# Kernel tuning notes

Hardware: AMD Instinct MI355X
Metric: run time of the kernel (lower is better)

The kernel has to match this reference:

```python
import jax, jax.numpy as jnp
import numpy as np
from jax import lax

N = 100000      # nodes
F_IN = 128      # dataset.num_features
H = 64          # hidden
E = 1600000     # edges
G = 1000        # graphs (equal-sized, contiguous)
PER = N // G    # nodes per graph = 100
K = 30          # sort-pool k
KS = 3          # conv1d kernel = num_layers


def setup_inputs() -> dict:
    key = jax.random.key(0)
    ks = jax.random.split(key, 20)
    lin = lambda k, i, o: (jax.random.normal(k, (i, o), jnp.float32) / np.sqrt(i)).astype(jnp.float32)
    return {
        "x": jax.random.normal(ks[0], (N, F_IN), jnp.float32),
        "src": jax.random.randint(ks[1], (E,), 0, N, dtype=jnp.int32),
        "dst": jax.random.randint(ks[2], (E,), 0, N, dtype=jnp.int32),
        "num_graphs": G,
        # SAGEConv 1: lin_l (aggr, with bias), lin_r (self, no bias)
        "wl1": lin(ks[3], F_IN, H), "wr1": lin(ks[4], F_IN, H), "b1": jnp.zeros((H,), jnp.float32),
        "wl2": lin(ks[5], H, H), "wr2": lin(ks[6], H, H), "b2": jnp.zeros((H,), jnp.float32),
        "wl3": lin(ks[7], H, H), "wr3": lin(ks[8], H, H), "b3": jnp.zeros((H,), jnp.float32),
        # Conv1d(hidden=64 -> 32, kernel=3): weight [O, I, K]
        "cw": (jax.random.normal(ks[9], (32, H, KS), jnp.float32) / np.sqrt(H * KS)).astype(jnp.float32),
        "cb": jnp.zeros((32,), jnp.float32),
        "w1": lin(ks[10], 32 * (K - KS + 1), H), "bb1": jnp.zeros((H,), jnp.float32),
        "w2": lin(ks[11], H, 1), "bb2": jnp.zeros((1,), jnp.float32),
    }


def _sage(x, src, dst, wl, wr, b, n):
    # PyG SAGEConv (mean aggr): lin_l(mean_{j->i} x_j) + lin_r(x_i)
    msum = jax.ops.segment_sum(x[src], dst, num_segments=n)           # [N, F]
    cnt = jax.ops.segment_sum(jnp.ones((src.shape[0],), x.dtype), dst, num_segments=n)
    mean = msum / jnp.maximum(cnt, 1.0)[:, None]
    return mean @ wl + b + x @ wr


def reference(x, src, dst, num_graphs, wl1, wr1, b1, wl2, wr2, b2, wl3, wr3, b3, cw, cb, w1, bb1, w2, bb2):
    n = x.shape[0]
    h = jax.nn.relu(_sage(x, src, dst, wl1, wr1, b1, n))
    h = jax.nn.relu(_sage(h, src, dst, wl2, wr2, b2, n))
    h = jax.nn.relu(_sage(h, src, dst, wl3, wr3, b3, n))
    # SortAggregation(k): per-graph, sort nodes by last feature channel (desc), keep top-k.
    # batch = contiguous equal-sized graphs -> dense reshape is exact.
    hg = h.reshape(num_graphs, PER, H)                                # [G, PER, H]
    order = jnp.argsort(-hg[:, :, -1], axis=1)[:, :K]                 # [G, K]
    topk = jnp.take_along_axis(hg, order[:, :, None], axis=1)         # [G, K, H]
    xc = jnp.transpose(topk, (0, 2, 1))                               # [G, H, K]
    y = lax.conv_general_dilated(xc, cw, (1,), 'VALID',
                                 dimension_numbers=('NCH', 'OIH', 'NCH'))
    y = jax.nn.relu(y + cb[None, :, None])                            # [G, 32, K-KS+1]
    y = y.reshape(num_graphs, -1)
    y = jax.nn.relu(y @ w1 + bb1)
    # dropout: eval mode -> identity
    return y @ w2 + bb2                                               # [G, 1]
```

## Files before the change

### kernel.cpp

```cpp
#include <hip/hip_runtime.h>

#define NN 100000
#define EE 1600000
#define GG 1000
#define PERG 100
#define KK 30
#define HH 64

#define NB 782
#define CAP 4096
#define CHB 4096
#define BUCKET_BLOCKS ((EE + CHB - 1) / CHB)
#define PROJ_BLOCKS ((NN + 127) / 128)

__global__ __launch_bounds__(1024) void zero_int(int* p, int n) {
  int i = blockIdx.x * 1024 + threadIdx.x;
  if (i < n) p[i] = 0;
}

__device__ __forceinline__ void bucket_body(int bid, float* smem,
                                            const int* __restrict__ src,
                                            const int* __restrict__ dst,
                                            int* __restrict__ gcur,
                                            int* __restrict__ pairs) {
  int* lhist = (int*)smem;
  int* lbase = lhist + NB;
  int* lcur = lbase + NB;
  const int t = threadIdx.x;
  const int c0 = bid * CHB;
  const int c1 = min(c0 + CHB, EE);
  for (int b = t; b < NB; b += 256) {
    lhist[b] = 0;
    lcur[b] = 0;
  }
  __syncthreads();
  for (int e = c0 + t; e < c1; e += 256) atomicAdd(&lhist[dst[e] >> 7], 1);
  __syncthreads();
  for (int b = t; b < NB; b += 256) {
    int c = lhist[b];
    lbase[b] = c ? atomicAdd(&gcur[b], c) : 0;
  }
  __syncthreads();
  for (int e = c0 + t; e < c1; e += 256) {
    int d = dst[e];
    int b = d >> 7;
    int p = atomicAdd(&lcur[b], 1);
    pairs[b * CAP + lbase[b] + p] = (src[e] << 7) | (d & 127);
  }
}

template <int K>
__device__ __forceinline__ void proj_body(int bid, float* smem,
                                          const float* __restrict__ X,
                                          const float* __restrict__ WL,
                                          const float* __restrict__ WR,
                                          float* __restrict__ P,
                                          float* __restrict__ R) {
  constexpr int BM = 128, BK = 32, XSP = 40, WSP = 144;
  float* xs = smem;
  float* ws = smem + BM * XSP;
  const int t = threadIdx.x;
  const int row0 = bid * BM;
  const int tc = t & 15, tr = t >> 4;
  const int wcol = tc * 8 + (tc >> 2) * 4;

  float acc[8][8];
#pragma unroll
  for (int i = 0; i < 8; ++i)
#pragma unroll
    for (int j = 0; j < 8; ++j) acc[i][j] = 0.f;

  for (int k0 = 0; k0 < K; k0 += BK) {
    __syncthreads();
    for (int idx = t; idx < BM * 8; idx += 256) {
      int r = idx >> 3, c = idx & 7;
      int row = row0 + r;
      float4 v = make_float4(0.f, 0.f, 0.f, 0.f);
      if (row < NN) v = *reinterpret_cast<const float4*>(&X[(size_t)row * K + k0 + c * 4]);
      *reinterpret_cast<float4*>(&xs[r * XSP + c * 4]) = v;
    }
    for (int idx = t; idx < BK * 16; idx += 256) {
      int kr = idx >> 4, c4 = idx & 15;
      int gcl = c4 >> 1;
      int off = gcl * 8 + (gcl >> 2) * 4 + (c4 & 1) * 4;
      *reinterpret_cast<float4*>(&ws[kr * WSP + off]) =
          *reinterpret_cast<const float4*>(&WL[(k0 + kr) * 64 + c4 * 4]);
      int g2 = gcl + 8;
      int off2 = g2 * 8 + (g2 >> 2) * 4 + (c4 & 1) * 4;
      *reinterpret_cast<float4*>(&ws[kr * WSP + off2]) =
          *reinterpret_cast<const float4*>(&WR[(k0 + kr) * 64 + c4 * 4]);
    }
    __syncthreads();
    for (int kk4 = 0; kk4 < BK; kk4 += 4) {
      float4 a[8];
#pragma unroll
      for (int i = 0; i < 8; ++i)
        a[i] = *reinterpret_cast<const float4*>(&xs[(tr + 16 * i) * XSP + kk4]);
#pragma unroll
      for (int kk = 0; kk < 4; ++kk) {
        float4 b0 = *reinterpret_cast<const float4*>(&ws[(kk4 + kk) * WSP + wcol]);
        float4 b1 = *reinterpret_cast<const float4*>(&ws[(kk4 + kk) * WSP + wcol + 4]);
        float bv[8] = {b0.x, b0.y, b0.z, b0.w, b1.x, b1.y, b1.z, b1.w};
#pragma unroll
        for (int i = 0; i < 8; ++i) {
          float av = (kk == 0) ? a[i].x : (kk == 1) ? a[i].y : (kk == 2) ? a[i].z : a[i].w;
#pragma unroll
          for (int j = 0; j < 8; ++j) acc[i][j] = fmaf(av, bv[j], acc[i][j]);
        }
      }
    }
  }

  float* OUT = (tc < 8) ? P : R;
  int cb = (tc & 7) * 8;
#pragma unroll
  for (int i = 0; i < 8; ++i) {
    int row = row0 + tr + 16 * i;
    if (row < NN) {
      *reinterpret_cast<float4*>(&OUT[(size_t)row * 64 + cb]) =
          make_float4(acc[i][0], acc[i][1], acc[i][2], acc[i][3]);
      *reinterpret_cast<float4*>(&OUT[(size_t)row * 64 + cb + 4]) =
          make_float4(acc[i][4], acc[i][5], acc[i][6], acc[i][7]);
    }
  }
}

__global__ __launch_bounds__(256) void fused_bucket_proj(const int* __restrict__ src,
                                                         const int* __restrict__ dst,
                                                         int* __restrict__ gcur,
                                                         int* __restrict__ pairs,
                                                         const float* __restrict__ X,
                                                         const float* __restrict__ WL,
                                                         const float* __restrict__ WR,
                                                         float* __restrict__ P,
                                                         float* __restrict__ R) {
  __shared__ float smem[128 * 40 + 32 * 144];
  if (blockIdx.x < BUCKET_BLOCKS)
    bucket_body(blockIdx.x, smem, src, dst, gcur, pairs);
  else
    proj_body<128>(blockIdx.x - BUCKET_BLOCKS, smem, X, WL, WR, P, R);
}

template <int K>
__global__ __launch_bounds__(256) void proj_kernel(const float* __restrict__ X,
                                                   const float* __restrict__ WL,
                                                   const float* __restrict__ WR,
                                                   float* __restrict__ P,
                                                   float* __restrict__ R) {
  __shared__ float smem[128 * 40 + 32 * 144];
  proj_body<K>(blockIdx.x, smem, X, WL, WR, P, R);
}

__global__ __launch_bounds__(256) void csr_kernel(const int* __restrict__ gcur,
                                                  const int* __restrict__ pairs,
                                                  int* __restrict__ row_start,
                                                  int* __restrict__ cnt,
                                                  int* __restrict__ eidx) {
  __shared__ int vals[CAP];
  __shared__ int hist[128];
  __shared__ int offs[128];
  __shared__ int cur[128];
  __shared__ int red[4];
  const int b = blockIdx.x;
  const int t = threadIdx.x;
  int s = 0;
  for (int i = t; i < b; i += 256) s += gcur[i];
#pragma unroll
  for (int off = 32; off > 0; off >>= 1) s += __shfl_xor(s, off);
  if ((t & 63) == 0) red[t >> 6] = s;
  if (t < 128) {
    hist[t] = 0;
    cur[t] = 0;
  }
  __syncthreads();
  const int base = red[0] + red[1] + red[2] + red[3];
  const int nb = gcur[b];
  for (int i = t; i < nb; i += 256) {
    int v = pairs[b * CAP + i];
    vals[i] = v;
    atomicAdd(&hist[v & 127], 1);
  }
  __syncthreads();
  if (t < 128) {
    int ss = 0;
    for (int m = 0; m < t; ++m) ss += hist[m];
    offs[t] = ss;
    int node = b * 128 + t;
    if (node < NN) {
      row_start[node] = base + ss;
      cnt[node] = hist[t];
    }
  }
  __syncthreads();
  for (int i = t; i < nb; i += 256) {
    int v = vals[i];
    int ld = v & 127;
    int p = atomicAdd(&cur[ld], 1);
    eidx[base + offs[ld] + p] = v >> 7;
  }
}

__global__ __launch_bounds__(256) void agg_kernel(const float* __restrict__ P,
                                                  const float* __restrict__ R,
                                                  const float* __restrict__ bias,
                                                  const int* __restrict__ row_start,
                                                  const int* __restrict__ cnt,
                                                  const int* __restrict__ eidx,
                                                  float* __restrict__ h,
                                                  float* __restrict__ keys) {
  int wid = (blockIdx.x * 256 + threadIdx.x) >> 6;
  int lane = threadIdx.x & 63;
  if (wid >= NN) return;
  const int q = lane >> 4;
  const int ql = lane & 15;
  const int base = row_start[wid];
  const int deg = cnt[wid];
  float4 a0 = make_float4(0.f, 0.f, 0.f, 0.f);
  float4 a1 = make_float4(0.f, 0.f, 0.f, 0.f);

  for (int e0 = 0; e0 < deg; e0 += 64) {
    const int m = min(64, deg - e0);
    int idx = (lane < m) ? eidx[base + e0 + lane] : 0;
    for (int j = 0; j < m; j += 16) {
      const int eA = j + q, eB = j + 4 + q, eC = j + 8 + q, eD = j + 12 + q;
      const int sA = __shfl(idx, min(eA, m - 1));
      const int sB = __shfl(idx, min(eB, m - 1));
      const int sC = __shfl(idx, min(eC, m - 1));
      const int sD = __shfl(idx, min(eD, m - 1));
      const float wA = (eA < m) ? 1.f : 0.f;
      const float wB = (eB < m) ? 1.f : 0.f;
      const float wC = (eC < m) ? 1.f : 0.f;
      const float wD = (eD < m) ? 1.f : 0.f;
      float4 vA = *reinterpret_cast<const float4*>(&P[(size_t)sA * 64 + ql * 4]);
      float4 vB = *reinterpret_cast<const float4*>(&P[(size_t)sB * 64 + ql * 4]);
      float4 vC = *reinterpret_cast<const float4*>(&P[(size_t)sC * 64 + ql * 4]);
      float4 vD = *reinterpret_cast<const float4*>(&P[(size_t)sD * 64 + ql * 4]);
      a0.x = fmaf(wA, vA.x, a0.x); a0.y = fmaf(wA, vA.y, a0.y);
      a0.z = fmaf(wA, vA.z, a0.z); a0.w = fmaf(wA, vA.w, a0.w);
      a1.x = fmaf(wB, vB.x, a1.x); a1.y = fmaf(wB, vB.y, a1.y);
      a1.z = fmaf(wB, vB.z, a1.z); a1.w = fmaf(wB, vB.w, a1.w);
      a0.x = fmaf(wC, vC.x, a0.x); a0.y = fmaf(wC, vC.y, a0.y);
      a0.z = fmaf(wC, vC.z, a0.z); a0.w = fmaf(wC, vC.w, a0.w);
      a1.x = fmaf(wD, vD.x, a1.x); a1.y = fmaf(wD, vD.y, a1.y);
      a1.z = fmaf(wD, vD.z, a1.z); a1.w = fmaf(wD, vD.w, a1.w);
    }
  }

  float4 acc = make_float4(a0.x + a1.x, a0.y + a1.y, a0.z + a1.z, a0.w + a1.w);
#pragma unroll
  for (int d = 16; d < 64; d <<= 1) {
    acc.x += __shfl_xor(acc.x, d);
    acc.y += __shfl_xor(acc.y, d);
    acc.z += __shfl_xor(acc.z, d);
    acc.w += __shfl_xor(acc.w, d);
  }

  if (q == 0) {
    const float dv = fmaxf((float)deg, 1.0f);
    float4 r4 = *reinterpret_cast<const float4*>(&R[(size_t)wid * 64 + ql * 4]);
    float4 b4 = *reinterpret_cast<const float4*>(&bias[ql * 4]);
    float4 o;
    o.x = fmaxf(acc.x / dv + b4.x + r4.x, 0.f);
    o.y = fmaxf(acc.y / dv + b4.y + r4.y, 0.f);
    o.z = fmaxf(acc.z / dv + b4.z + r4.z, 0.f);
    o.w = fmaxf(acc.w / dv + b4.w + r4.w, 0.f);
    *reinterpret_cast<float4*>(&h[(size_t)wid * 64 + ql * 4]) = o;
    if (keys != nullptr && ql == 15) keys[wid] = o.w;
  }
}

__global__ __launch_bounds__(256) void head_kernel(const float* __restrict__ h,
                                                   const float* __restrict__ keysArr,
                                                   const float* __restrict__ cw,
                                                   const float* __restrict__ cb,
                                                   const float* __restrict__ w1,
                                                   const float* __restrict__ bb1,
                                                   const float* __restrict__ w2,
                                                   const float* __restrict__ bb2,
                                                   float* __restrict__ out) {
  __shared__ float key[PERG];
  __shared__ int sel[KK];
  __shared__ float feat[34 * 65];
  __shared__ float cwT[192 * 33];
  __shared__ float z[896];
  __shared__ float psum[256];
  const int g = blockIdx.x;
  const int t = threadIdx.x;

  for (int idx = t; idx < 32 * 192; idx += 256) {
    int o = idx / 192, k = idx % 192;
    cwT[k * 33 + o] = cw[idx];
  }
  if (t < PERG) key[t] = keysArr[g * PERG + t];
  __syncthreads();

  if (t < PERG) {
    float kv = key[t];
    int r = 0;
    for (int m = 0; m < PERG; ++m) {
      float km = key[m];
      r += (int)((km > kv) || (km == kv && m < t));
    }
    if (r < KK) sel[r] = t;
  }
  __syncthreads();

  for (int idx = t; idx < KK * HH; idx += 256) {
    int r = idx >> 6, f = idx & 63;
    feat[r * 65 + f] = h[(size_t)(g * PERG + sel[r]) * HH + f];
  }
  __syncthreads();

  {
    const int o = t & 31;
    const int pg = t >> 5;
    float zacc[4] = {0.f, 0.f, 0.f, 0.f};
    int i = 0, tt = 0;
    for (int k = 0; k < 192; ++k) {
      float c = cwT[k * 33 + o];
#pragma unroll
      for (int j = 0; j < 4; ++j) {
        int p = pg + 8 * j;
        zacc[j] = fmaf(c, feat[(p + tt) * 65 + i], zacc[j]);
      }
      if (++tt == 3) {
        tt = 0;
        ++i;
      }
    }
    float cbo = cb[o];
#pragma unroll
    for (int j = 0; j < 4; ++j) {
      int p = pg + 8 * j;
      if (p < 28) z[o * 28 + p] = fmaxf(zacc[j] + cbo, 0.f);
    }
  }
  __syncthreads();

  {
    const int hh = t & 63;
    const int quarter = t >> 6;
    const int q0 = quarter * 224;
    float acc = 0.f;
    for (int q = 0; q < 224; ++q)
      acc = fmaf(z[q0 + q], w1[(size_t)(q0 + q) * 64 + hh], acc);
    psum[t] = acc;
  }
  __syncthreads();

  if (t < 64) {
    float o1 = fmaxf(bb1[t] + psum[t] + psum[t + 64] + psum[t + 128] + psum[t + 192], 0.f);
    float v = o1 * w2[t];
#pragma unroll
    for (int off = 32; off > 0; off >>= 1) v += __shfl_down(v, off);
    if (t == 0) out[g] = v + bb2[0];
  }
}

extern "C" void kernel_launch(void* const* d_in, const int* in_sizes, int n_in,
                              void* d_out, int out_size, void* d_ws, size_t ws_size,
                              hipStream_t stream) {
  const float* x = (const float*)d_in[0];
  const int* src = (const int*)d_in[1];
  const int* dst = (const int*)d_in[2];
  const float* wl1 = (const float*)d_in[4];
  const float* wr1 = (const float*)d_in[5];
  const float* b1 = (const float*)d_in[6];
  const float* wl2 = (const float*)d_in[7];
  const float* wr2 = (const float*)d_in[8];
  const float* b2 = (const float*)d_in[9];
  const float* wl3 = (const float*)d_in[10];
  const float* wr3 = (const float*)d_in[11];
  const float* b3 = (const float*)d_in[12];
  const float* cw = (const float*)d_in[13];
  const float* cb = (const float*)d_in[14];
  const float* w1 = (const float*)d_in[15];
  const float* bb1 = (const float*)d_in[16];
  const float* w2 = (const float*)d_in[17];
  const float* bb2 = (const float*)d_in[18];
  float* out = (float*)d_out;

  char* w = (char*)d_ws;
  auto carve = [&](size_t bytes) {
    char* p = w;
    w += (bytes + 255) & ~(size_t)255;
    return p;
  };
  int* row_start = (int*)carve((size_t)NN * 4);
  int* cnt = (int*)carve((size_t)NN * 4);
  int* eidx = (int*)carve((size_t)EE * 4);
  float* P = (float*)carve((size_t)NN * 64 * 4);
  float* R = (float*)carve((size_t)NN * 64 * 4);
  float* hbuf = (float*)carve((size_t)NN * 64 * 4);
  float* keys = (float*)carve((size_t)NN * 4);
  int* gcur = (int*)carve((size_t)NB * 4);
  int* pairs = (int*)hbuf;

  zero_int<<<1, 1024, 0, stream>>>(gcur, NB);
  fused_bucket_proj<<<BUCKET_BLOCKS + PROJ_BLOCKS, 256, 0, stream>>>(
      src, dst, gcur, pairs, x, wl1, wr1, P, R);
  csr_kernel<<<NB, 256, 0, stream>>>(gcur, pairs, row_start, cnt, eidx);

  const int aggGrid = (NN + 3) / 4;
  agg_kernel<<<aggGrid, 256, 0, stream>>>(P, R, b1, row_start, cnt, eidx, hbuf, nullptr);
  proj_kernel<64><<<PROJ_BLOCKS, 256, 0, stream>>>(hbuf, wl2, wr2, P, R);
  agg_kernel<<<aggGrid, 256, 0, stream>>>(P, R, b2, row_start, cnt, eidx, hbuf, nullptr);
  proj_kernel<64><<<PROJ_BLOCKS, 256, 0, stream>>>(hbuf, wl3, wr3, P, R);
  agg_kernel<<<aggGrid, 256, 0, stream>>>(P, R, b3, row_start, cnt, eidx, hbuf, keys);
  head_kernel<<<GG, 256, 0, stream>>>(hbuf, keys, cw, cb, w1, bb1, w2, bb2, out);
}
```

Baseline: 488.4 us.

## Process four nodes per wavefront in aggregation and reorder fused launch blocks

The mean-aggregation kernel now gives each 16-lane quarter of a wavefront its own destination node, instead of one node per wavefront with a cross-quarter shuffle reduction. This removes the final xor-reduction, cuts idle lanes for low-degree nodes (average degree is 16), and quarters the grid size. The fused bucket/projection kernel now schedules projection blocks first. The zeroing kernel is replaced with hipMemsetAsync. Quarters within a wave can diverge when node degrees differ, and each quarter's 16-edge loop pads partial chunks with zero-weighted loads.

```diff
diff --git a/kernel.cpp b/kernel.cpp
--- a/kernel.cpp
+++ b/kernel.cpp
@@ -12,11 +12,6 @@
 #define CHB 4096
 #define BUCKET_BLOCKS ((EE + CHB - 1) / CHB)
 #define PROJ_BLOCKS ((NN + 127) / 128)
-
-__global__ __launch_bounds__(1024) void zero_int(int* p, int n) {
-  int i = blockIdx.x * 1024 + threadIdx.x;
-  if (i < n) p[i] = 0;
-}
 
 __device__ __forceinline__ void bucket_body(int bid, float* smem,
                                             const int* __restrict__ src,
@@ -135,10 +130,10 @@
                                                          float* __restrict__ P,
                                                          float* __restrict__ R) {
   __shared__ float smem[128 * 40 + 32 * 144];
-  if (blockIdx.x < BUCKET_BLOCKS)
-    bucket_body(blockIdx.x, smem, src, dst, gcur, pairs);
+  if (blockIdx.x < PROJ_BLOCKS)
+    proj_body<128>(blockIdx.x, smem, X, WL, WR, P, R);
   else
-    proj_body<128>(blockIdx.x - BUCKET_BLOCKS, smem, X, WL, WR, P, R);
+    bucket_body(blockIdx.x - PROJ_BLOCKS, smem, src, dst, gcur, pairs);
 }
 
 template <int K>
@@ -208,65 +203,42 @@
                                                   const int* __restrict__ eidx,
                                                   float* __restrict__ h,
                                                   float* __restrict__ keys) {
-  int wid = (blockIdx.x * 256 + threadIdx.x) >> 6;
-  int lane = threadIdx.x & 63;
-  if (wid >= NN) return;
+  const int wv = (blockIdx.x * 256 + threadIdx.x) >> 6;
+  const int lane = threadIdx.x & 63;
   const int q = lane >> 4;
   const int ql = lane & 15;
-  const int base = row_start[wid];
-  const int deg = cnt[wid];
-  float4 a0 = make_float4(0.f, 0.f, 0.f, 0.f);
-  float4 a1 = make_float4(0.f, 0.f, 0.f, 0.f);
-
-  for (int e0 = 0; e0 < deg; e0 += 64) {
-    const int m = min(64, deg - e0);
-    int idx = (lane < m) ? eidx[base + e0 + lane] : 0;
-    for (int j = 0; j < m; j += 16) {
-      const int eA = j + q, eB = j + 4 + q, eC = j + 8 + q, eD = j + 12 + q;
-      const int sA = __shfl(idx, min(eA, m - 1));
-      const int sB = __shfl(idx, min(eB, m - 1));
-      const int sC = __shfl(idx, min(eC, m - 1));
-      const int sD = __shfl(idx, min(eD, m - 1));
-      const float wA = (eA < m) ? 1.f : 0.f;
-      const float wB = (eB < m) ? 1.f : 0.f;
-      const float wC = (eC < m) ? 1.f : 0.f;
-      const float wD = (eD < m) ? 1.f : 0.f;
-      float4 vA = *reinterpret_cast<const float4*>(&P[(size_t)sA * 64 + ql * 4]);
-      float4 vB = *reinterpret_cast<const float4*>(&P[(size_t)sB * 64 + ql * 4]);
-      float4 vC = *reinterpret_cast<const float4*>(&P[(size_t)sC * 64 + ql * 4]);
-      float4 vD = *reinterpret_cast<const float4*>(&P[(size_t)sD * 64 + ql * 4]);
-      a0.x = fmaf(wA, vA.x, a0.x); a0.y = fmaf(wA, vA.y, a0.y);
-      a0.z = fmaf(wA, vA.z, a0.z); a0.w = fmaf(wA, vA.w, a0.w);
-      a1.x = fmaf(wB, vB.x, a1.x); a1.y = fmaf(wB, vB.y, a1.y);
-      a1.z = fmaf(wB, vB.z, a1.z); a1.w = fmaf(wB, vB.w, a1.w);
-      a0.x = fmaf(wC, vC.x, a0.x); a0.y = fmaf(wC, vC.y, a0.y);
-      a0.z = fmaf(wC, vC.z, a0.z); a0.w = fmaf(wC, vC.w, a0.w);
-      a1.x = fmaf(wD, vD.x, a1.x); a1.y = fmaf(wD, vD.y, a1.y);
-      a1.z = fmaf(wD, vD.z, a1.z); a1.w = fmaf(wD, vD.w, a1.w);
-    }
-  }
-
-  float4 acc = make_float4(a0.x + a1.x, a0.y + a1.y, a0.z + a1.z, a0.w + a1.w);
-#pragma unroll
-  for (int d = 16; d < 64; d <<= 1) {
-    acc.x += __shfl_xor(acc.x, d);
-    acc.y += __shfl_xor(acc.y, d);
-    acc.z += __shfl_xor(acc.z, d);
-    acc.w += __shfl_xor(acc.w, d);
-  }
-
-  if (q == 0) {
-    const float dv = fmaxf((float)deg, 1.0f);
-    float4 r4 = *reinterpret_cast<const float4*>(&R[(size_t)wid * 64 + ql * 4]);
-    float4 b4 = *reinterpret_cast<const float4*>(&bias[ql * 4]);
-    float4 o;
-    o.x = fmaxf(acc.x / dv + b4.x + r4.x, 0.f);
-    o.y = fmaxf(acc.y / dv + b4.y + r4.y, 0.f);
-    o.z = fmaxf(acc.z / dv + b4.z + r4.z, 0.f);
-    o.w = fmaxf(acc.w / dv + b4.w + r4.w, 0.f);
-    *reinterpret_cast<float4*>(&h[(size_t)wid * 64 + ql * 4]) = o;
-    if (keys != nullptr && ql == 15) keys[wid] = o.w;
-  }
+  const int node = wv * 4 + q;
+  if (node >= NN) return;
+  const int base = row_start[node];
+  const int deg = cnt[node];
+  float4 acc = make_float4(0.f, 0.f, 0.f, 0.f);
+
+  for (int e0 = 0; e0 < deg; e0 += 16) {
+    const int rem = deg - e0;
+    const int ii = (ql < rem) ? ql : (rem - 1);
+    int idx = eidx[base + e0 + ii];
+#pragma unroll
+    for (int j = 0; j < 16; ++j) {
+      const int sj = __shfl(idx, (lane & 48) | j);
+      const float wj = (j < rem) ? 1.f : 0.f;
+      const float4 vj = *reinterpret_cast<const float4*>(&P[(size_t)sj * 64 + ql * 4]);
+      acc.x = fmaf(wj, vj.x, acc.x);
+      acc.y = fmaf(wj, vj.y, acc.y);
+      acc.z = fmaf(wj, vj.z, acc.z);
+      acc.w = fmaf(wj, vj.w, acc.w);
+    }
+  }
+
+  const float dv = fmaxf((float)deg, 1.0f);
+  float4 r4 = *reinterpret_cast<const float4*>(&R[(size_t)node * 64 + ql * 4]);
+  float4 b4 = *reinterpret_cast<const float4*>(&bias[ql * 4]);
+  float4 o;
+  o.x = fmaxf(acc.x / dv + b4.x + r4.x, 0.f);
+  o.y = fmaxf(acc.y / dv + b4.y + r4.y, 0.f);
+  o.z = fmaxf(acc.z / dv + b4.z + r4.z, 0.f);
+  o.w = fmaxf(acc.w / dv + b4.w + r4.w, 0.f);
+  *reinterpret_cast<float4*>(&h[(size_t)node * 64 + ql * 4]) = o;
+  if (keys != nullptr && ql == 15) keys[node] = o.w;
 }
 
 __global__ __launch_bounds__(256) void head_kernel(const float* __restrict__ h,
@@ -396,12 +368,12 @@
   int* gcur = (int*)carve((size_t)NB * 4);
   int* pairs = (int*)hbuf;
 
-  zero_int<<<1, 1024, 0, stream>>>(gcur, NB);
+  hipMemsetAsync(gcur, 0, (size_t)NB * 4, stream);
   fused_bucket_proj<<<BUCKET_BLOCKS + PROJ_BLOCKS, 256, 0, stream>>>(
       src, dst, gcur, pairs, x, wl1, wr1, P, R);
   csr_kernel<<<NB, 256, 0, stream>>>(gcur, pairs, row_start, cnt, eidx);
 
-  const int aggGrid = (NN + 3) / 4;
+  const int aggGrid = (NN + 15) / 16;
   agg_kernel<<<aggGrid, 256, 0, stream>>>(P, R, b1, row_start, cnt, eidx, hbuf, nullptr);
   proj_kernel<64><<<PROJ_BLOCKS, 256, 0, stream>>>(hbuf, wl2, wr2, P, R);
   agg_kernel<<<aggGrid, 256, 0, stream>>>(P, R, b2, row_start, cnt, eidx, hbuf, nullptr);
```

Measured after the change: 497.0 us. Within noise of the previous version (+1.8%).
